# Kernel tuning notes

Hardware: AMD Instinct MI355X
Metric: run time of the kernel (lower is better)

The kernel has to match this reference:

```python
import jax, jax.numpy as jnp
import numpy as np

N_NODES = 100000
N_TYPES = 7
E_PER_TYPE = 250000
D = 128


def setup_inputs() -> dict:
    key = jax.random.key(0)
    k1, k2, k3 = jax.random.split(key, 3)
    x = jax.random.normal(k1, (N_NODES, D), dtype=jnp.float32)
    edge_index = jax.random.randint(k2, (N_TYPES, 2, E_PER_TYPE), 0, N_NODES, dtype=jnp.int64)
    # per-edge-type GNN weights (SwitchModule holds one param set per type)
    W = jax.random.normal(k3, (N_TYPES, D, D), dtype=jnp.float32) * (1.0 / np.sqrt(D))
    b = jnp.zeros((N_TYPES, D), dtype=jnp.float32)
    return {"x": x, "edge_index": edge_index, "W": W, "b": b}


def reference(x, edge_index, W, b):
    # x: [N, D]; edge_index: [T, 2, E]; W: [T, D, D]; b: [T, D]
    N = x.shape[0]
    E = edge_index.shape[-1]
    # per-type linear transform of all node features: [T, N, D]
    h = jnp.einsum('nd,tdf->tnf', x, W) + b[:, None, :]

    def per_type(ht, ei):
        src, dst = ei[0], ei[1]
        msgs = ht[src]                                   # [E, D] gather
        sums = jax.ops.segment_sum(msgs, dst, num_segments=N)
        cnt = jax.ops.segment_sum(jnp.ones((E,), ht.dtype), dst, num_segments=N)
        return sums / jnp.maximum(cnt, 1.0)[:, None]     # mean aggregation

    type_messages = jax.vmap(per_type)(h, edge_index)    # [T, N, D]
    # x_agg = sum(type_messages) / len(type_messages)
    return type_messages.mean(axis=0)
```

## Files before the change

### kernel.cpp

```cpp
#include <hip/hip_runtime.h>


constexpr int NN = 100000;
constexpr int NT = 7;
constexpr int NE = 250000;
constexpr int DD = 128;
constexpr int CAP = 20;
constexpr int OVF = CAP - 8;
constexpr int NROWS = ((NN + 127) / 128) * 128;
constexpr int NPART = 8;
constexpr int PSIZE = (NN + NPART - 1) / NPART;
constexpr int EPB = 1024;
constexpr int NSLAB = (NE + EPB - 1) / EPB;

typedef short bf16x8 __attribute__((ext_vector_type(8)));
typedef float f32x4 __attribute__((ext_vector_type(4)));
typedef int   i32x4 __attribute__((ext_vector_type(4)));
typedef float fltx4 __attribute__((ext_vector_type(4)));

__device__ __forceinline__ unsigned pack_bf16x2(float lo, float hi) {
    unsigned a = __float_as_uint(lo), b = __float_as_uint(hi);
    unsigned al = (a + 0x7FFFu + ((a >> 16) & 1u)) >> 16;
    unsigned bh = (b + 0x7FFFu + ((b >> 16) & 1u)) & 0xFFFF0000u;
    return al | bh;
}

__global__ __launch_bounds__(256) void convx_k(
    const float* __restrict__ x, uint4* __restrict__ xb)
{
    int id = blockIdx.x * 256 + threadIdx.x;
    const fltx4* src = (const fltx4*)x;
    fltx4 v0 = __builtin_nontemporal_load(src + (size_t)id * 2);
    fltx4 v1 = __builtin_nontemporal_load(src + (size_t)id * 2 + 1);
    uint4 o;
    o.x = pack_bf16x2(v0[0], v0[1]);
    o.y = pack_bf16x2(v0[2], v0[3]);
    o.z = pack_bf16x2(v1[0], v1[1]);
    o.w = pack_bf16x2(v1[2], v1[3]);
    xb[id] = o;
}

__global__ __launch_bounds__(256) void wconv_k(
    const float* __restrict__ W, char* __restrict__ WTb)
{
    int wid = (blockIdx.x * 256 + threadIdx.x) >> 6;
    int lane = threadIdx.x & 63;
    int t = wid >> 7, f = wid & 127;
    if (t >= NT) return;
    const float* Wt = W + (size_t)t * DD * DD;
    float w0 = Wt[(size_t)(2 * lane) * DD + f];
    float w1 = Wt[(size_t)(2 * lane + 1) * DD + f];
    int gran = (lane >> 2) ^ (f & 7);
    *(unsigned*)(WTb + (size_t)t * 32768 + f * 256 + gran * 16 + (lane & 3) * 4)
        = pack_bf16x2(w0, w1);
}

__global__ __launch_bounds__(256) void fill_k(
    const int* __restrict__ ei,
    int* __restrict__ cnt,
    int* __restrict__ eidx8,
    int* __restrict__ ovf)
{
    int part = blockIdx.x & (NPART - 1);
    int slab = blockIdx.x >> 3;
    int t = blockIdx.y;
    int e0 = slab * EPB + threadIdx.x * 4;
    if (e0 >= NE) return;
    const int* p = ei + (size_t)t * 2 * NE;
    i32x4 s4 = __builtin_nontemporal_load((const i32x4*)(p + e0));
    i32x4 d4 = __builtin_nontemporal_load((const i32x4*)(p + NE + e0));
    int lo = part * PSIZE;
    int hi = lo + PSIZE;
    #pragma unroll
    for (int k = 0; k < 4; ++k) {
        int src = s4[k];
        int dst = d4[k];
        if (dst >= lo && dst < hi) {
            int pos = atomicAdd(cnt + (size_t)dst * NT + t, 1);
            if (pos < 8)        eidx8[((size_t)dst * NT + t) * 8 + pos] = src;
            else if (pos < CAP) ovf[((size_t)t * NN + dst) * OVF + (pos - 8)] = src;
        }
    }
}

__global__ __launch_bounds__(256) void agg_k(
    const char* __restrict__ xb,
    const int* __restrict__ cnt,
    const int* __restrict__ eidx8,
    const int* __restrict__ ovf,
    char* __restrict__ aggb,
    int c0, int nc)
{
    int wid = (blockIdx.x * 256 + threadIdx.x) >> 6;
    int lane = threadIdx.x & 63;
    if (wid >= nc) return;
    const int n = c0 + wid;
    const bool live = (n < NN);

    int cntv = (live && lane < NT)
             ? __builtin_nontemporal_load(cnt + (size_t)n * NT + lane) : 0;
    int idxv = (live && lane < 56)
             ? __builtin_nontemporal_load(eidx8 + (size_t)n * 56 + lane) : 0;

    int r = wid & 127;
    int gran = (lane >> 2) ^ (r & 7);
    char* wbase = aggb + (size_t)(wid >> 7) * 32768 + r * 256
                + gran * 16 + (lane & 3) * 4;
    const size_t tstride = (size_t)nc * 256;

    for (int tp = 0; tp < NT; tp += 2) {
        int cA = __shfl(cntv, tp);
        int cB = (tp + 1 < NT) ? __shfl(cntv, tp + 1) : 0;
        int ccA = cA < CAP ? cA : CAP;
        int ccB = cB < CAP ? cB : CAP;
        int m = ccA > ccB ? ccA : ccB;

        float a0 = 0.f, a1 = 0.f, b0 = 0.f, b1 = 0.f;
        for (int e = 0; e < m; e += 2) {
            unsigned vA0 = 0, vA1 = 0, vB0 = 0, vB1 = 0;
            bool gA0 = e < ccA, gA1 = e + 1 < ccA;
            bool gB0 = e < ccB, gB1 = e + 1 < ccB;
            if (gA0) {
                int s = (e < 8) ? __shfl(idxv, tp * 8 + e)
                                : __builtin_nontemporal_load(
                                      ovf + ((size_t)tp * NN + n) * OVF + (e - 8));
                vA0 = *(const unsigned*)(xb + (size_t)s * 256 + lane * 4);
            }
            if (gA1) {
                int s = (e + 1 < 8) ? __shfl(idxv, tp * 8 + e + 1)
                                    : __builtin_nontemporal_load(
                                          ovf + ((size_t)tp * NN + n) * OVF + (e - 7));
                vA1 = *(const unsigned*)(xb + (size_t)s * 256 + lane * 4);
            }
            if (gB0) {
                int s = (e < 8) ? __shfl(idxv, (tp + 1) * 8 + e)
                                : __builtin_nontemporal_load(
                                      ovf + ((size_t)(tp + 1) * NN + n) * OVF + (e - 8));
                vB0 = *(const unsigned*)(xb + (size_t)s * 256 + lane * 4);
            }
            if (gB1) {
                int s = (e + 1 < 8) ? __shfl(idxv, (tp + 1) * 8 + e + 1)
                                    : __builtin_nontemporal_load(
                                          ovf + ((size_t)(tp + 1) * NN + n) * OVF + (e - 7));
                vB1 = *(const unsigned*)(xb + (size_t)s * 256 + lane * 4);
            }
            a0 += __uint_as_float(vA0 << 16) + __uint_as_float(vA1 << 16);
            a1 += __uint_as_float(vA0 & 0xFFFF0000u) + __uint_as_float(vA1 & 0xFFFF0000u);
            b0 += __uint_as_float(vB0 << 16) + __uint_as_float(vB1 << 16);
            b1 += __uint_as_float(vB0 & 0xFFFF0000u) + __uint_as_float(vB1 & 0xFFFF0000u);
        }
        float sa = 1.0f / fmaxf((float)cA, 1.0f);
        *(unsigned*)(wbase + (size_t)tp * tstride) = pack_bf16x2(a0 * sa, a1 * sa);
        if (tp + 1 < NT) {
            float sb = 1.0f / fmaxf((float)cB, 1.0f);
            *(unsigned*)(wbase + (size_t)(tp + 1) * tstride) = pack_bf16x2(b0 * sb, b1 * sb);
        }
    }
}

__global__ __launch_bounds__(512) void gemm_k(
    const char* __restrict__ aggb, const char* __restrict__ WTb,
    const int* __restrict__ cnt, const float* __restrict__ bias,
    float* __restrict__ out, int c0, int nc)
{
    __shared__ char sA[128 * 256];
    __shared__ char sW[128 * 256];
    int tid = threadIdx.x;
    int w = tid >> 6, lane = tid & 63;
    int wy = w >> 1, wx = w & 1;
    int n0 = c0 + blockIdx.x * 128;
    const size_t tstride = (size_t)nc * 256;

    f32x4 acc[2][4];
    #pragma unroll
    for (int i = 0; i < 2; ++i)
        #pragma unroll
        for (int j = 0; j < 4; ++j) acc[i][j] = (f32x4)0.0f;

    for (int t = 0; t < NT; ++t) {
        __syncthreads();
        const char* asrc = aggb + (size_t)t * tstride + (size_t)blockIdx.x * 32768;
        const char* wsrc = WTb + (size_t)t * 32768;
        #pragma unroll
        for (int i = 0; i < 4; ++i) {
            int ch = w * 4 + i;
            __builtin_amdgcn_global_load_lds(
                (const __attribute__((address_space(1))) void*)(asrc + ch * 1024 + lane * 16),
                (__attribute__((address_space(3))) void*)(sA + ch * 1024), 16, 0, 0);
            __builtin_amdgcn_global_load_lds(
                (const __attribute__((address_space(1))) void*)(wsrc + ch * 1024 + lane * 16),
                (__attribute__((address_space(3))) void*)(sW + ch * 1024), 16, 0, 0);
        }
        __syncthreads();

        #pragma unroll
        for (int c = 0; c < 4; ++c) {
            int gsel = ((c * 4 + (lane >> 4)) ^ (lane & 7)) << 4;
            bf16x8 A0 = *(const bf16x8*)(sA + (wy * 32 + (lane & 15)) * 256 + gsel);
            bf16x8 A1 = *(const bf16x8*)(sA + (wy * 32 + 16 + (lane & 15)) * 256 + gsel);
            #pragma unroll
            for (int nj = 0; nj < 4; ++nj) {
                bf16x8 B = *(const bf16x8*)(sW + (wx * 64 + nj * 16 + (lane & 15)) * 256 + gsel);
                acc[0][nj] = __builtin_amdgcn_mfma_f32_16x16x32_bf16(A0, B, acc[0][nj], 0, 0, 0);
                acc[1][nj] = __builtin_amdgcn_mfma_f32_16x16x32_bf16(A1, B, acc[1][nj], 0, 0, 0);
            }
        }
    }

    const float inv7 = 1.0f / (float)NT;
    #pragma unroll
    for (int mi = 0; mi < 2; ++mi) {
        #pragma unroll
        for (int v = 0; v < 4; ++v) {
            int n = n0 + wy * 32 + mi * 16 + (lane >> 4) * 4 + v;
            if (n >= NN) continue;
            float add[4] = {0.f, 0.f, 0.f, 0.f};
            for (int t = 0; t < NT; ++t) {
                if (cnt[(size_t)n * NT + t] > 0) {
                    #pragma unroll
                    for (int nj = 0; nj < 4; ++nj)
                        add[nj] += bias[(size_t)t * DD + wx * 64 + nj * 16 + (lane & 15)];
                }
            }
            #pragma unroll
            for (int nj = 0; nj < 4; ++nj)
                out[(size_t)n * DD + wx * 64 + nj * 16 + (lane & 15)]
                    = inv7 * (acc[mi][nj][v] + add[nj]);
        }
    }
}

extern "C" void kernel_launch(void* const* d_in, const int* in_sizes, int n_in,
                              void* d_out, int out_size, void* d_ws, size_t ws_size,
                              hipStream_t stream) {
    const float* x  = (const float*)d_in[0];
    const int*   ei = (const int*)d_in[1];
    const float* W  = (const float*)d_in[2];
    const float* b  = (const float*)d_in[3];
    float* out = (float*)d_out;
    char* ws = (char*)d_ws;

    size_t off = 0;
    char* xb    = ws + off; off += (size_t)NN * 256;
    char* WTb   = ws + off; off += (size_t)NT * 128 * 256;
    int*  eidx8 = (int*)(ws + off); off += (size_t)NN * NT * 8 * 4;
    int*  cnti  = (int*)(ws + off); off += (size_t)NN * NT * 4;
    int*  ovfp  = (int*)(ws + off); off += (size_t)NT * NN * OVF * 4;
    char* aggb  = ws + off;

    size_t avail = (ws_size > off) ? (ws_size - off) : 0;
    int Nc = (int)(avail / ((size_t)NT * 256));
    Nc &= ~127;
    if (Nc < 128) Nc = 128;
    if (Nc > NROWS) Nc = NROWS;

    convx_k<<<(NN * DD / 8 + 255) / 256, 256, 0, stream>>>(x, (uint4*)xb);
    wconv_k<<<(NT * 128 + 3) / 4, 256, 0, stream>>>(W, WTb);
    hipMemsetAsync(cnti, 0, (size_t)NN * NT * 4, stream);
    fill_k<<<dim3(NSLAB * NPART, NT), 256, 0, stream>>>(ei, cnti, eidx8, ovfp);

    for (int c0 = 0; c0 < NN; c0 += Nc) {
        int nc = (NROWS - c0 < Nc) ? (NROWS - c0) : Nc;
        agg_k<<<nc / 4, 256, 0, stream>>>(xb, cnti, eidx8, ovfp, aggb, c0, nc);
        gemm_k<<<nc / 128, 512, 0, stream>>>(aggb, WTb, cnti, b, out, c0, nc);
    }
}
```

Before: 264.2 us.

## Double-buffer gemm_k LDS staging in half-K steps and pack aggregation adds

gemm_k now splits each edge type's 128-wide K dimension into two 64-wide halves, giving 14 stages. It double-buffers these halves in LDS, so the global-to-LDS loads for the next stage overlap the MFMA work on the current one. A manual `s_waitcnt vmcnt(4)` plus barrier replaces the full syncthreads pair. The aggregation kernel accumulates into f32x2 vectors, which may allow packed FP32 adds, and writes its bf16 results with nontemporal stores. In exchange the swizzle and addressing logic become more intricate, and there are more barriers per type.

```diff
diff --git a/kernel.cpp b/kernel.cpp
--- a/kernel.cpp
+++ b/kernel.cpp
@@ -15,6 +15,7 @@
 
 typedef short bf16x8 __attribute__((ext_vector_type(8)));
 typedef float f32x4 __attribute__((ext_vector_type(4)));
+typedef float f32x2 __attribute__((ext_vector_type(2)));
 typedef int   i32x4 __attribute__((ext_vector_type(4)));
 typedef float fltx4 __attribute__((ext_vector_type(4)));
 
@@ -115,45 +116,45 @@
         int ccB = cB < CAP ? cB : CAP;
         int m = ccA > ccB ? ccA : ccB;
 
-        float a0 = 0.f, a1 = 0.f, b0 = 0.f, b1 = 0.f;
+        f32x2 aA = {0.f, 0.f}, aB = {0.f, 0.f};
         for (int e = 0; e < m; e += 2) {
             unsigned vA0 = 0, vA1 = 0, vB0 = 0, vB1 = 0;
-            bool gA0 = e < ccA, gA1 = e + 1 < ccA;
-            bool gB0 = e < ccB, gB1 = e + 1 < ccB;
-            if (gA0) {
+            if (e < ccA) {
                 int s = (e < 8) ? __shfl(idxv, tp * 8 + e)
                                 : __builtin_nontemporal_load(
                                       ovf + ((size_t)tp * NN + n) * OVF + (e - 8));
                 vA0 = *(const unsigned*)(xb + (size_t)s * 256 + lane * 4);
             }
-            if (gA1) {
+            if (e + 1 < ccA) {
                 int s = (e + 1 < 8) ? __shfl(idxv, tp * 8 + e + 1)
                                     : __builtin_nontemporal_load(
                                           ovf + ((size_t)tp * NN + n) * OVF + (e - 7));
                 vA1 = *(const unsigned*)(xb + (size_t)s * 256 + lane * 4);
             }
-            if (gB0) {
+            if (e < ccB) {
                 int s = (e < 8) ? __shfl(idxv, (tp + 1) * 8 + e)
                                 : __builtin_nontemporal_load(
                                       ovf + ((size_t)(tp + 1) * NN + n) * OVF + (e - 8));
                 vB0 = *(const unsigned*)(xb + (size_t)s * 256 + lane * 4);
             }
-            if (gB1) {
+            if (e + 1 < ccB) {
                 int s = (e + 1 < 8) ? __shfl(idxv, (tp + 1) * 8 + e + 1)
                                     : __builtin_nontemporal_load(
                                           ovf + ((size_t)(tp + 1) * NN + n) * OVF + (e - 7));
                 vB1 = *(const unsigned*)(xb + (size_t)s * 256 + lane * 4);
             }
-            a0 += __uint_as_float(vA0 << 16) + __uint_as_float(vA1 << 16);
-            a1 += __uint_as_float(vA0 & 0xFFFF0000u) + __uint_as_float(vA1 & 0xFFFF0000u);
-            b0 += __uint_as_float(vB0 << 16) + __uint_as_float(vB1 << 16);
-            b1 += __uint_as_float(vB0 & 0xFFFF0000u) + __uint_as_float(vB1 & 0xFFFF0000u);
+            aA += (f32x2){__uint_as_float(vA0 << 16), __uint_as_float(vA0 & 0xFFFF0000u)};
+            aA += (f32x2){__uint_as_float(vA1 << 16), __uint_as_float(vA1 & 0xFFFF0000u)};
+            aB += (f32x2){__uint_as_float(vB0 << 16), __uint_as_float(vB0 & 0xFFFF0000u)};
+            aB += (f32x2){__uint_as_float(vB1 << 16), __uint_as_float(vB1 & 0xFFFF0000u)};
         }
         float sa = 1.0f / fmaxf((float)cA, 1.0f);
-        *(unsigned*)(wbase + (size_t)tp * tstride) = pack_bf16x2(a0 * sa, a1 * sa);
+        __builtin_nontemporal_store(pack_bf16x2(aA[0] * sa, aA[1] * sa),
+                                    (unsigned*)(wbase + (size_t)tp * tstride));
         if (tp + 1 < NT) {
             float sb = 1.0f / fmaxf((float)cB, 1.0f);
-            *(unsigned*)(wbase + (size_t)(tp + 1) * tstride) = pack_bf16x2(b0 * sb, b1 * sb);
+            __builtin_nontemporal_store(pack_bf16x2(aB[0] * sb, aB[1] * sb),
+                                        (unsigned*)(wbase + (size_t)(tp + 1) * tstride));
         }
     }
 }
@@ -163,13 +164,15 @@
     const int* __restrict__ cnt, const float* __restrict__ bias,
     float* __restrict__ out, int c0, int nc)
 {
-    __shared__ char sA[128 * 256];
-    __shared__ char sW[128 * 256];
+    __shared__ char sA[2 * 16384];
+    __shared__ char sW[2 * 16384];
     int tid = threadIdx.x;
     int w = tid >> 6, lane = tid & 63;
     int wy = w >> 1, wx = w & 1;
     int n0 = c0 + blockIdx.x * 128;
     const size_t tstride = (size_t)nc * 256;
+    const char* abase0 = aggb + (size_t)blockIdx.x * 32768;
+    const int ro = (lane >> 3) * 256 + (lane & 7) * 16;
 
     f32x4 acc[2][4];
     #pragma unroll
@@ -177,34 +180,48 @@
         #pragma unroll
         for (int j = 0; j < 4; ++j) acc[i][j] = (f32x4)0.0f;
 
-    for (int t = 0; t < NT; ++t) {
-        __syncthreads();
-        const char* asrc = aggb + (size_t)t * tstride + (size_t)blockIdx.x * 32768;
-        const char* wsrc = WTb + (size_t)t * 32768;
-        #pragma unroll
-        for (int i = 0; i < 4; ++i) {
-            int ch = w * 4 + i;
+    auto stage = [&](int buf, int ss) {
+        int t = ss >> 1, h = ss & 1;
+        const char* ab = abase0 + (size_t)t * tstride + h * 128;
+        const char* wb = WTb + (size_t)t * 32768 + h * 128;
+        #pragma unroll
+        for (int i = 0; i < 2; ++i) {
+            int ch = w * 2 + i;
             __builtin_amdgcn_global_load_lds(
-                (const __attribute__((address_space(1))) void*)(asrc + ch * 1024 + lane * 16),
-                (__attribute__((address_space(3))) void*)(sA + ch * 1024), 16, 0, 0);
+                (const __attribute__((address_space(1))) void*)(ab + ch * 2048 + ro),
+                (__attribute__((address_space(3))) void*)(sA + buf * 16384 + ch * 1024),
+                16, 0, 0);
             __builtin_amdgcn_global_load_lds(
-                (const __attribute__((address_space(1))) void*)(wsrc + ch * 1024 + lane * 16),
-                (__attribute__((address_space(3))) void*)(sW + ch * 1024), 16, 0, 0);
-        }
-        __syncthreads();
-
-        #pragma unroll
-        for (int c = 0; c < 4; ++c) {
-            int gsel = ((c * 4 + (lane >> 4)) ^ (lane & 7)) << 4;
-            bf16x8 A0 = *(const bf16x8*)(sA + (wy * 32 + (lane & 15)) * 256 + gsel);
-            bf16x8 A1 = *(const bf16x8*)(sA + (wy * 32 + 16 + (lane & 15)) * 256 + gsel);
+                (const __attribute__((address_space(1))) void*)(wb + ch * 2048 + ro),
+                (__attribute__((address_space(3))) void*)(sW + buf * 16384 + ch * 1024),
+                16, 0, 0);
+        }
+    };
+
+    stage(0, 0);
+    #pragma unroll
+    for (int s = 0; s < 14; ++s) {
+        if (s < 13) {
+            stage((s + 1) & 1, s + 1);
+            asm volatile("s_waitcnt vmcnt(4)\n\ts_barrier" ::: "memory");
+        } else {
+            asm volatile("s_waitcnt vmcnt(0)\n\ts_barrier" ::: "memory");
+        }
+        const char* As = sA + (s & 1) * 16384;
+        const char* Ws = sW + (s & 1) * 16384;
+        #pragma unroll
+        for (int cl = 0; cl < 2; ++cl) {
+            int gsel = ((cl * 4 + (lane >> 4)) ^ (lane & 7)) << 4;
+            bf16x8 A0 = *(const bf16x8*)(As + (wy * 32 + (lane & 15)) * 128 + gsel);
+            bf16x8 A1 = *(const bf16x8*)(As + (wy * 32 + 16 + (lane & 15)) * 128 + gsel);
             #pragma unroll
             for (int nj = 0; nj < 4; ++nj) {
-                bf16x8 B = *(const bf16x8*)(sW + (wx * 64 + nj * 16 + (lane & 15)) * 256 + gsel);
+                bf16x8 B = *(const bf16x8*)(Ws + (wx * 64 + nj * 16 + (lane & 15)) * 128 + gsel);
                 acc[0][nj] = __builtin_amdgcn_mfma_f32_16x16x32_bf16(A0, B, acc[0][nj], 0, 0, 0);
                 acc[1][nj] = __builtin_amdgcn_mfma_f32_16x16x32_bf16(A1, B, acc[1][nj], 0, 0, 0);
             }
         }
+        __builtin_amdgcn_s_barrier();
     }
 
     const float inv7 = 1.0f / (float)NT;
```

Result: slower. 277.4 us (+5.0%).

## Pad edge slots with zero-row sentinel, branchless gather, smaller GEMM tiles

Applied to the files above, without the earlier changes.

Edge index slots are pre-filled with a sentinel pointing at an extra zero row appended to the bf16 feature table. This lets the aggregation loop issue its first eight gathers per type unconditionally, with no per-edge branches, and handles overflow edges in a separate loop. The GEMM is retiled to 64-row blocks of 256 threads that stage K in two halves, cutting LDS use so more blocks fit per CU, and the aggregation output layout is changed to match. The cost is an extra init kernel that writes the whole eidx8 array, plus wasted loads of the zero row for nodes with fewer than eight edges.

```diff
diff --git a/kernel.cpp b/kernel.cpp
--- a/kernel.cpp
+++ b/kernel.cpp
@@ -53,6 +53,12 @@
     int gran = (lane >> 2) ^ (f & 7);
     *(unsigned*)(WTb + (size_t)t * 32768 + f * 256 + gran * 16 + (lane & 3) * 4)
         = pack_bf16x2(w0, w1);
+}
+
+__global__ __launch_bounds__(256) void init_k(int* __restrict__ eidx8)
+{
+    int id = blockIdx.x * 256 + threadIdx.x;
+    if (id < NN * NT * 8) eidx8[id] = NN;
 }
 
 __global__ __launch_bounds__(256) void fill_k(
@@ -100,11 +106,10 @@
     int cntv = (live && lane < NT)
              ? __builtin_nontemporal_load(cnt + (size_t)n * NT + lane) : 0;
     int idxv = (live && lane < 56)
-             ? __builtin_nontemporal_load(eidx8 + (size_t)n * 56 + lane) : 0;
-
-    int r = wid & 127;
-    int gran = (lane >> 2) ^ (r & 7);
-    char* wbase = aggb + (size_t)(wid >> 7) * 32768 + r * 256
+             ? __builtin_nontemporal_load(eidx8 + (size_t)n * 56 + lane) : NN;
+
+    int gran = (lane >> 2) ^ (wid & 7);
+    char* wbase = aggb + (size_t)(wid >> 6) * 16384 + (wid & 63) * 256
                 + gran * 16 + (lane & 3) * 4;
     const size_t tstride = (size_t)nc * 256;
 
@@ -114,40 +119,40 @@
         int ccA = cA < CAP ? cA : CAP;
         int ccB = cB < CAP ? cB : CAP;
         int m = ccA > ccB ? ccA : ccB;
+        int mm = m < 8 ? m : 8;
 
         float a0 = 0.f, a1 = 0.f, b0 = 0.f, b1 = 0.f;
-        for (int e = 0; e < m; e += 2) {
-            unsigned vA0 = 0, vA1 = 0, vB0 = 0, vB1 = 0;
-            bool gA0 = e < ccA, gA1 = e + 1 < ccA;
-            bool gB0 = e < ccB, gB1 = e + 1 < ccB;
-            if (gA0) {
-                int s = (e < 8) ? __shfl(idxv, tp * 8 + e)
-                                : __builtin_nontemporal_load(
-                                      ovf + ((size_t)tp * NN + n) * OVF + (e - 8));
-                vA0 = *(const unsigned*)(xb + (size_t)s * 256 + lane * 4);
-            }
-            if (gA1) {
-                int s = (e + 1 < 8) ? __shfl(idxv, tp * 8 + e + 1)
-                                    : __builtin_nontemporal_load(
-                                          ovf + ((size_t)tp * NN + n) * OVF + (e - 7));
-                vA1 = *(const unsigned*)(xb + (size_t)s * 256 + lane * 4);
-            }
-            if (gB0) {
-                int s = (e < 8) ? __shfl(idxv, (tp + 1) * 8 + e)
-                                : __builtin_nontemporal_load(
-                                      ovf + ((size_t)(tp + 1) * NN + n) * OVF + (e - 8));
-                vB0 = *(const unsigned*)(xb + (size_t)s * 256 + lane * 4);
-            }
-            if (gB1) {
-                int s = (e + 1 < 8) ? __shfl(idxv, (tp + 1) * 8 + e + 1)
-                                    : __builtin_nontemporal_load(
-                                          ovf + ((size_t)(tp + 1) * NN + n) * OVF + (e - 7));
-                vB1 = *(const unsigned*)(xb + (size_t)s * 256 + lane * 4);
-            }
+        for (int e = 0; e < mm; e += 2) {
+            int sA0 = __shfl(idxv, tp * 8 + e);
+            int sA1 = __shfl(idxv, tp * 8 + e + 1);
+            int sB0 = __shfl(idxv, tp * 8 + 8 + e);
+            int sB1 = __shfl(idxv, tp * 8 + 9 + e);
+            unsigned vA0 = *(const unsigned*)(xb + (size_t)sA0 * 256 + lane * 4);
+            unsigned vA1 = *(const unsigned*)(xb + (size_t)sA1 * 256 + lane * 4);
+            unsigned vB0 = *(const unsigned*)(xb + (size_t)sB0 * 256 + lane * 4);
+            unsigned vB1 = *(const unsigned*)(xb + (size_t)sB1 * 256 + lane * 4);
             a0 += __uint_as_float(vA0 << 16) + __uint_as_float(vA1 << 16);
             a1 += __uint_as_float(vA0 & 0xFFFF0000u) + __uint_as_float(vA1 & 0xFFFF0000u);
             b0 += __uint_as_float(vB0 << 16) + __uint_as_float(vB1 << 16);
             b1 += __uint_as_float(vB0 & 0xFFFF0000u) + __uint_as_float(vB1 & 0xFFFF0000u);
+        }
+        if (m > 8) {
+            for (int e = 8; e < m; ++e) {
+                if (e < ccA) {
+                    int s = __builtin_nontemporal_load(
+                        ovf + ((size_t)tp * NN + n) * OVF + (e - 8));
+                    unsigned v = *(const unsigned*)(xb + (size_t)s * 256 + lane * 4);
+                    a0 += __uint_as_float(v << 16);
+                    a1 += __uint_as_float(v & 0xFFFF0000u);
+                }
+                if (e < ccB) {
+                    int s = __builtin_nontemporal_load(
+                        ovf + ((size_t)(tp + 1) * NN + n) * OVF + (e - 8));
+                    unsigned v = *(const unsigned*)(xb + (size_t)s * 256 + lane * 4);
+                    b0 += __uint_as_float(v << 16);
+                    b1 += __uint_as_float(v & 0xFFFF0000u);
+                }
+            }
         }
         float sa = 1.0f / fmaxf((float)cA, 1.0f);
         *(unsigned*)(wbase + (size_t)tp * tstride) = pack_bf16x2(a0 * sa, a1 * sa);
@@ -158,18 +163,20 @@
     }
 }
 
-__global__ __launch_bounds__(512) void gemm_k(
+__global__ __launch_bounds__(256, 5) void gemm_k(
     const char* __restrict__ aggb, const char* __restrict__ WTb,
     const int* __restrict__ cnt, const float* __restrict__ bias,
     float* __restrict__ out, int c0, int nc)
 {
-    __shared__ char sA[128 * 256];
-    __shared__ char sW[128 * 256];
+    __shared__ char sA[64 * 128];
+    __shared__ char sW[128 * 128];
     int tid = threadIdx.x;
     int w = tid >> 6, lane = tid & 63;
     int wy = w >> 1, wx = w & 1;
-    int n0 = c0 + blockIdx.x * 128;
+    int n0 = c0 + blockIdx.x * 64;
     const size_t tstride = (size_t)nc * 256;
+    const char* abase0 = aggb + (size_t)blockIdx.x * 16384;
+    const int ro = (lane >> 3) * 256 + (lane & 7) * 16;
 
     f32x4 acc[2][4];
     #pragma unroll
@@ -177,30 +184,35 @@
         #pragma unroll
         for (int j = 0; j < 4; ++j) acc[i][j] = (f32x4)0.0f;
 
-    for (int t = 0; t < NT; ++t) {
+    for (int s = 0; s < 14; ++s) {
+        int t = s >> 1, h = s & 1;
         __syncthreads();
-        const char* asrc = aggb + (size_t)t * tstride + (size_t)blockIdx.x * 32768;
-        const char* wsrc = WTb + (size_t)t * 32768;
+        const char* ab = abase0 + (size_t)t * tstride + h * 128;
+        const char* wb = WTb + (size_t)t * 32768 + h * 128;
+        #pragma unroll
+        for (int i = 0; i < 2; ++i) {
+            int ch = w * 2 + i;
+            __builtin_amdgcn_global_load_lds(
+                (const __attribute__((address_space(1))) void*)(ab + ch * 2048 + ro),
+                (__attribute__((address_space(3))) void*)(sA + ch * 1024), 16, 0, 0);
+        }
         #pragma unroll
         for (int i = 0; i < 4; ++i) {
             int ch = w * 4 + i;
             __builtin_amdgcn_global_load_lds(
-                (const __attribute__((address_space(1))) void*)(asrc + ch * 1024 + lane * 16),
-                (__attribute__((address_space(3))) void*)(sA + ch * 1024), 16, 0, 0);
-            __builtin_amdgcn_global_load_lds(
-                (const __attribute__((address_space(1))) void*)(wsrc + ch * 1024 + lane * 16),
+                (const __attribute__((address_space(1))) void*)(wb + ch * 2048 + ro),
                 (__attribute__((address_space(3))) void*)(sW + ch * 1024), 16, 0, 0);
         }
         __syncthreads();
 
         #pragma unroll
-        for (int c = 0; c < 4; ++c) {
-            int gsel = ((c * 4 + (lane >> 4)) ^ (lane & 7)) << 4;
-            bf16x8 A0 = *(const bf16x8*)(sA + (wy * 32 + (lane & 15)) * 256 + gsel);
-            bf16x8 A1 = *(const bf16x8*)(sA + (wy * 32 + 16 + (lane & 15)) * 256 + gsel);
+        for (int cl = 0; cl < 2; ++cl) {
+            int gsel = ((cl * 4 + (lane >> 4)) ^ (lane & 7)) << 4;
+            bf16x8 A0 = *(const bf16x8*)(sA + (wy * 32 + (lane & 15)) * 128 + gsel);
+            bf16x8 A1 = *(const bf16x8*)(sA + (wy * 32 + 16 + (lane & 15)) * 128 + gsel);
             #pragma unroll
             for (int nj = 0; nj < 4; ++nj) {
-                bf16x8 B = *(const bf16x8*)(sW + (wx * 64 + nj * 16 + (lane & 15)) * 256 + gsel);
+                bf16x8 B = *(const bf16x8*)(sW + (wx * 64 + nj * 16 + (lane & 15)) * 128 + gsel);
                 acc[0][nj] = __builtin_amdgcn_mfma_f32_16x16x32_bf16(A0, B, acc[0][nj], 0, 0, 0);
                 acc[1][nj] = __builtin_amdgcn_mfma_f32_16x16x32_bf16(A1, B, acc[1][nj], 0, 0, 0);
             }
@@ -241,7 +253,7 @@
     char* ws = (char*)d_ws;
 
     size_t off = 0;
-    char* xb    = ws + off; off += (size_t)NN * 256;
+    char* xb    = ws + off; off += (size_t)(NN + 1) * 256;
     char* WTb   = ws + off; off += (size_t)NT * 128 * 256;
     int*  eidx8 = (int*)(ws + off); off += (size_t)NN * NT * 8 * 4;
     int*  cnti  = (int*)(ws + off); off += (size_t)NN * NT * 4;
@@ -255,13 +267,15 @@
     if (Nc > NROWS) Nc = NROWS;
 
     convx_k<<<(NN * DD / 8 + 255) / 256, 256, 0, stream>>>(x, (uint4*)xb);
+    hipMemsetAsync(xb + (size_t)NN * 256, 0, 256, stream);
     wconv_k<<<(NT * 128 + 3) / 4, 256, 0, stream>>>(W, WTb);
     hipMemsetAsync(cnti, 0, (size_t)NN * NT * 4, stream);
+    init_k<<<(NN * NT * 8 + 255) / 256, 256, 0, stream>>>(eidx8);
     fill_k<<<dim3(NSLAB * NPART, NT), 256, 0, stream>>>(ei, cnti, eidx8, ovfp);
 
     for (int c0 = 0; c0 < NN; c0 += Nc) {
         int nc = (NROWS - c0 < Nc) ? (NROWS - c0) : Nc;
         agg_k<<<nc / 4, 256, 0, stream>>>(xb, cnti, eidx8, ovfp, aggb, c0, nc);
-        gemm_k<<<nc / 128, 512, 0, stream>>>(aggb, WTb, cnti, b, out, c0, nc);
-    }
-}
+        gemm_k<<<nc / 64, 256, 0, stream>>>(aggb, WTb, cnti, b, out, c0, nc);
+    }
+}
```

New measurement: 270.9 us. 1.03x slower.
